# Kernel tuning notes

Measured on AMD Instinct MI355X. Metric: run time of the kernel, lower is better.

Reference implementation:

```python
import jax, jax.numpy as jnp
import numpy as np
import math

B, T, C, H = 4, 2048, 1024, 16
HD = C // H  # head dim = 64


def setup_inputs() -> dict:
    key = jax.random.key(0)
    ks = jax.random.split(key, 8)
    s = 0.02
    x = jax.random.normal(ks[0], (B, T, C), dtype=jnp.float32)
    Wq = jax.random.normal(ks[1], (C, C), dtype=jnp.float32) * s
    bq = jnp.zeros((C,), dtype=jnp.float32)
    Wkv = jax.random.normal(ks[2], (C, 2 * C), dtype=jnp.float32) * s
    bkv = jnp.zeros((2 * C,), dtype=jnp.float32)
    Wp = jax.random.normal(ks[3], (C, C), dtype=jnp.float32) * s
    bp = jnp.zeros((C,), dtype=jnp.float32)
    # ALiBi slopes: m_h = 2^(-8*(h+1)/H), shape [H,1,1] to broadcast over [B,H,T,T]
    slopes = 2.0 ** (-8.0 * (jnp.arange(1, H + 1, dtype=jnp.float32) / H))
    alibi_m = slopes.reshape(H, 1, 1)
    # relative-position offset table: offset[i,j] = -(i-j) for j<=i, 0 elsewhere
    i = jnp.arange(T)[:, None]
    j = jnp.arange(T)[None, :]
    alibi_offset = jnp.where(j <= i, (j - i).astype(jnp.float32), 0.0)
    return {"x": x, "Wq": Wq, "bq": bq, "Wkv": Wkv, "bkv": bkv,
            "Wp": Wp, "bp": bp, "alibi_m": alibi_m, "alibi_offset": alibi_offset}


def reference(x, Wq, bq, Wkv, bkv, Wp, bp, alibi_m, alibi_offset):
    Bq, Tq, Cq = x.shape
    q = x @ Wq + bq                                  # [B,T,C]
    kv = x @ Wkv + bkv                               # [B,T,2C]
    k, v = jnp.split(kv, 2, axis=-1)
    q = q.reshape(Bq, Tq, H, HD).transpose(0, 2, 1, 3)  # [B,H,T,hd]
    k = k.reshape(Bq, Tq, H, HD).transpose(0, 2, 1, 3)
    v = v.reshape(Bq, Tq, H, HD).transpose(0, 2, 1, 3)
    att = jnp.einsum('bhqd,bhkd->bhqk', q, k) / math.sqrt(HD)  # [B,H,T,T]
    att = att + alibi_m * alibi_offset[:Tq, :Tq]
    causal = jnp.tril(jnp.ones((Tq, Tq), dtype=bool))
    att = jnp.where(causal, att, -jnp.inf)
    att = jax.nn.softmax(att, axis=-1)
    y = jnp.einsum('bhqk,bhkd->bhqd', att, v)        # [B,H,T,hd]
    y = y.transpose(0, 2, 1, 3).reshape(Bq, Tq, Cq)
    y = y @ Wp + bp
    return y
```

## Files before the change

### kernel.cpp

```cpp
#include <hip/hip_runtime.h>
#include <hip/hip_bf16.h>
#include <math.h>

typedef __bf16 bf16_t;
typedef bf16_t bf16x8 __attribute__((ext_vector_type(8)));
typedef bf16_t bf16x4 __attribute__((ext_vector_type(4)));
typedef float  f32x4  __attribute__((ext_vector_type(4)));

#define MFMA_16x16x32_BF16(a, b, c) __builtin_amdgcn_mfma_f32_16x16x32_bf16((a), (b), (c), 0, 0, 0)

static constexpr int BB = 4, TT = 2048, CC = 1024, HH = 16, HD = 64;
static constexpr int C3 = 3 * CC;
static constexpr int MM = BB * TT;
static constexpr size_t SL = (size_t)BB * HH * TT * HD;

__device__ __forceinline__ float fast_exp2(float x) {
  float r;
  asm("v_exp_f32 %0, %1" : "=v"(r) : "v"(x));
  return r;
}

__device__ __forceinline__ void gload16(const void* g, void* l) {
  __builtin_amdgcn_global_load_lds(
      (const __attribute__((address_space(1))) unsigned int*)g,
      (__attribute__((address_space(3))) unsigned int*)l, 16, 0, 0);
}

__global__ void cast_x_kernel(const float* __restrict__ x, bf16_t* __restrict__ xb, int n4) {
  int i = blockIdx.x * blockDim.x + threadIdx.x;
  if (i >= n4) return;
  float4 v = reinterpret_cast<const float4*>(x)[i];
  bf16x4 o;
  o[0] = (bf16_t)v.x; o[1] = (bf16_t)v.y; o[2] = (bf16_t)v.z; o[3] = (bf16_t)v.w;
  reinterpret_cast<bf16x4*>(xb)[i] = o;
}

__global__ void transpose_cast_kernel(const float* __restrict__ in, bf16_t* __restrict__ out,
                                      int R, int Cn) {
  __shared__ float tile[32][33];
  int c0 = blockIdx.x * 32, r0 = blockIdx.y * 32;
  int tx = threadIdx.x, ty = threadIdx.y;
#pragma unroll
  for (int i = 0; i < 4; ++i)
    tile[ty + 8 * i][tx] = in[(size_t)(r0 + ty + 8 * i) * Cn + c0 + tx];
  __syncthreads();
#pragma unroll
  for (int i = 0; i < 4; ++i)
    out[(size_t)(c0 + ty + 8 * i) * R + r0 + tx] = (bf16_t)tile[tx][ty + 8 * i];
}

__global__ void transpose_v_kernel(const bf16_t* __restrict__ vh, bf16_t* __restrict__ vt) {
  __shared__ bf16_t tile[32][33];
  int t0 = blockIdx.x * 32, d0 = blockIdx.y * 32, bh = blockIdx.z;
  int tx = threadIdx.x, ty = threadIdx.y;
  const bf16_t* src = vh + (size_t)bh * TT * HD;
  bf16_t* dst = vt + (size_t)bh * TT * HD + (size_t)(t0 >> 5) * (HD * 32);
#pragma unroll
  for (int i = 0; i < 4; ++i)
    tile[ty + 8 * i][tx] = src[(size_t)(t0 + ty + 8 * i) * HD + d0 + tx];
  __syncthreads();
#pragma unroll
  for (int i = 0; i < 4; ++i)
    dst[(size_t)(d0 + ty + 8 * i) * 32 + tx] = tile[tx][ty + 8 * i];
}

__global__ void concat_bias_kernel(const float* __restrict__ bq, const float* __restrict__ bkv,
                                   float* __restrict__ dst) {
  int i = blockIdx.x * 256 + threadIdx.x;
  if (i >= 3072) return;
  const float* p = (i < 1024) ? (bq + i) : (bkv + i - 1024);
  dst[i] = *p;
}

__device__ inline void store_out(float* p, float v)  { *p = v; }
__device__ inline void store_out(bf16_t* p, float v) { *p = (bf16_t)v; }

template <int SPLIT, typename OutT>
__global__ __launch_bounds__(256) void gemm_kernel(
    const bf16_t* __restrict__ A, const bf16_t* __restrict__ Bt, OutT* __restrict__ C,
    const float* __restrict__ bias, int M, int N, int K, int gx, int cpx) {
  __shared__ bf16_t As[128][64];
  __shared__ bf16_t Bs[128][64];
  const int tid = threadIdx.x;
  const int wid = tid >> 6, lane = tid & 63;
  const int lhi = lane >> 4, llo = lane & 15;
  const int wm = (wid >> 1) * 64, wn = (wid & 1) * 64;
  const int bid = blockIdx.x;
  const int xcd = bid & 7, lb = bid >> 3;
  const int bandw = gx >> 3;
  const int bx = xcd * bandw + (lb % bandw);
  const int by = lb / bandw;
  const int m0 = bx * 128, n0 = by * 128;
  const int l8 = lane >> 3;
  const int s8 = ((lane & 7) ^ l8) * 8;

  const bf16_t* gA = A + (size_t)(m0 + wid * 32 + l8) * K + s8;
  const bf16_t* gB = Bt + (size_t)(n0 + wid * 32 + l8) * K + s8;
  bf16_t* lA = &As[wid * 32][0];
  bf16_t* lB = &Bs[wid * 32][0];
  const int rs0 = (lhi ^ (llo & 7)) * 16;

  f32x4 acc[4][4] = {};
  for (int k0 = 0; k0 < K; k0 += 64) {
    __syncthreads();
#pragma unroll
    for (int g = 0; g < 4; ++g) {
      gload16(gA + k0 + (size_t)(8 * g) * K, lA + 8 * g * 64);
      gload16(gB + k0 + (size_t)(8 * g) * K, lB + 8 * g * 64);
    }
    __syncthreads();
#pragma unroll
    for (int kk = 0; kk < 2; ++kk) {
      const int ro = rs0 ^ (kk * 64);
      bf16x8 af[4], bfr[4];
#pragma unroll
      for (int mi = 0; mi < 4; ++mi)
        af[mi] = *(const bf16x8*)((const char*)&As[wm + mi * 16 + llo][0] + ro);
#pragma unroll
      for (int ni = 0; ni < 4; ++ni)
        bfr[ni] = *(const bf16x8*)((const char*)&Bs[wn + ni * 16 + llo][0] + ro);
#pragma unroll
      for (int mi = 0; mi < 4; ++mi)
#pragma unroll
        for (int ni = 0; ni < 4; ++ni)
          acc[mi][ni] = MFMA_16x16x32_BF16(af[mi], bfr[ni], acc[mi][ni]);
    }
  }

#pragma unroll
  for (int mi = 0; mi < 4; ++mi) {
#pragma unroll
    for (int ni = 0; ni < 4; ++ni) {
      const int row0 = m0 + wm + mi * 16 + 4 * lhi;
      const int col  = n0 + wn + ni * 16 + llo;
      const float bv = bias[col];
      if constexpr (SPLIT) {
        const int sel = col >> 10, rem = col & 1023;
        const int hh = rem >> 6, dd = rem & 63;
#pragma unroll
        for (int r = 0; r < 4; ++r) {
          const int row = row0 + r;
          const int bb = row >> 11, t = row & 2047;
          size_t addr = ((((size_t)sel * BB + bb) * HH + hh) * TT + t) * HD + dd;
          ((bf16_t*)C)[addr] = (bf16_t)(acc[mi][ni][r] + bv);
        }
      } else {
#pragma unroll
        for (int r = 0; r < 4; ++r)
          store_out(&C[(size_t)(row0 + r) * N + col], acc[mi][ni][r] + bv);
      }
    }
  }
}

__global__ __launch_bounds__(256, 3) void attn_kernel(
    const bf16_t* __restrict__ qh,
    const bf16_t* __restrict__ kh,
    const bf16_t* __restrict__ vt,
    const float* __restrict__ alibi_m,
    bf16_t* __restrict__ y) {
  __shared__ bf16_t Klds[2][64][64];
  __shared__ bf16_t Vlds[2][2][64][32];
  __shared__ bf16_t Plds[4][32][68];
  const int tid = threadIdx.x, wid = tid >> 6, lane = tid & 63;
  const int lhi = lane >> 4, llo = lane & 15;
  const int bid = blockIdx.x;
  const int x = bid & 7, u = bid >> 3;
  const int b = u & 3, sel = (u >> 2) & 1, jtd = u >> 3;
  const int h = sel ? (15 - x) : x;
  const int jt = 15 - jtd;
  const int bh = b * HH + h;
  const int q0 = jt * 128 + wid * 32;

  const float mh2 = alibi_m[h] * 1.44269504f;
  const float C1 = 0.18033688f;
  const float M0 = 17.3f;
  const int Dwin = (int)(40.0f / mh2);

  const bf16_t* qbase = qh + (size_t)bh * TT * HD;
  const bf16_t* kbase = kh + (size_t)bh * TT * HD;
  const bf16_t* vbase = vt + (size_t)bh * TT * HD;

  float frm[2][4], w16c[4];
#pragma unroll
  for (int f = 0; f < 2; ++f)
#pragma unroll
    for (int r = 0; r < 4; ++r) frm[f][r] = (float)(16 * f + r) * mh2;
#pragma unroll
  for (int c = 0; c < 4; ++c) w16c[c] = fast_exp2((float)(16 * c) * mh2);

  const int l8 = lane >> 3;
  const size_t kst = (size_t)(wid * 8 + l8) * 64 + ((lane & 7) ^ l8) * 8;
  const int vf_st = ((lane >> 2) & 3) ^ ((lane >> 4) & 3);
  const size_t vst = (size_t)(wid * 16 + (lane >> 2)) * 32 + ((lane & 3) ^ vf_st) * 8;

#define STAGE(BUF, KV0)                                                          \
  do {                                                                           \
    const bf16_t* ks_ = kbase + (size_t)(KV0) * HD + kst;                        \
    bf16_t* kd_ = &Klds[BUF][0][0] + wid * 512;                                  \
    gload16(ks_, kd_);                                                           \
    gload16(ks_ + 2048, kd_ + 2048);                                             \
    const bf16_t* vs_ = vbase + ((size_t)((KV0) >> 5)) * 2048 + vst;             \
    bf16_t* vd_ = &Vlds[BUF][0][0][0] + wid * 512;                               \
    gload16(vs_, vd_);                                                           \
    gload16(vs_ + 2048, vd_ + 2048);                                             \
  } while (0)

  bf16x8 qf[2][2];
#pragma unroll
  for (int f = 0; f < 2; ++f) {
    const bf16_t* qp = qbase + (size_t)(q0 + 16 * f + llo) * HD + 8 * lhi;
    qf[f][0] = *(const bf16x8*)qp;
    qf[f][1] = *(const bf16x8*)(qp + 32);
  }

  f32x4 acc[2][4] = {};
  float lsum[2][4] = {};
  const float bias0 = mh2 * (float)(llo - 4 * lhi - q0) - M0;

  const int kvT = jt * 128;
  int ksm = kvT - Dwin; ksm = (ksm < 0) ? 0 : (ksm & ~63);
  const int nIter = (kvT - ksm) >> 6;

  if (nIter > 0) STAGE(0, ksm);
  __syncthreads();

  const int krd0 = (lhi ^ (llo & 7)) * 16;
  const int krd1 = ((4 + lhi) ^ (llo & 7)) * 16;
  const int vrd = (lhi ^ ((llo & 3) ^ ((llo >> 2) & 3))) * 16;

  int buf = 0;
#pragma unroll 1
  for (int it = 0; it < nIter; ++it) {
    const int kv0 = ksm + (it << 6);
    if (it + 1 < nIter) STAGE(buf ^ 1, kv0 + 64);
    const char* kb = (const char*)&Klds[buf][0][0];
    const char* vb = (const char*)&Vlds[buf][0][0][0];
    f32x4 s[2][4];
#pragma unroll
    for (int c = 0; c < 4; ++c) {
      bf16x8 k0 = *(const bf16x8*)(kb + (16 * c + llo) * 128 + krd0);
      bf16x8 k1 = *(const bf16x8*)(kb + (16 * c + llo) * 128 + krd1);
      s[0][c] = MFMA_16x16x32_BF16(qf[0][0], k0, f32x4{});
      s[0][c] = MFMA_16x16x32_BF16(qf[0][1], k1, s[0][c]);
      s[1][c] = MFMA_16x16x32_BF16(qf[1][0], k0, f32x4{});
      s[1][c] = MFMA_16x16x32_BF16(qf[1][1], k1, s[1][c]);
    }
    bf16x8 vv[4][2];
#pragma unroll
    for (int d = 0; d < 4; ++d) {
      vv[d][0] = *(const bf16x8*)(vb + (16 * d + llo) * 64 + vrd);
      vv[d][1] = *(const bf16x8*)(vb + 4096 + (16 * d + llo) * 64 + vrd);
    }
    const float tb0 = fmaf(mh2, (float)kv0, bias0);
#pragma unroll
    for (int f = 0; f < 2; ++f) {
#pragma unroll
      for (int r = 0; r < 4; ++r) {
        const float rb = tb0 - frm[f][r];
#pragma unroll
        for (int c = 0; c < 4; ++c) {
          float pv = fast_exp2(fmaf(s[f][c][r], C1, rb)) * w16c[c];
          lsum[f][r] += pv;
          Plds[wid][16 * f + 4 * lhi + r][16 * c + llo] = (bf16_t)pv;
        }
      }
    }
#pragma unroll
    for (int f = 0; f < 2; ++f) {
      const bf16x8 pa0 = *(const bf16x8*)&Plds[wid][16 * f + llo][8 * lhi];
      const bf16x8 pa1 = *(const bf16x8*)&Plds[wid][16 * f + llo][32 + 8 * lhi];
#pragma unroll
      for (int d = 0; d < 4; ++d) {
        acc[f][d] = MFMA_16x16x32_BF16(pa0, vv[d][0], acc[f][d]);
        acc[f][d] = MFMA_16x16x32_BF16(pa1, vv[d][1], acc[f][d]);
      }
    }
    __syncthreads();
    buf ^= 1;
  }

  const int tend = q0 & ~63;
#pragma unroll 1
  for (int kv0 = kvT; kv0 <= tend; kv0 += 64) {
    const int d31 = q0 + 31 - kv0;
    const int dbase = q0 + 4 * lhi - llo - kv0;
    f32x4 s[2][4];
#pragma unroll
    for (int c = 0; c < 4; ++c) {
      if (16 * c > d31) continue;
      const bf16_t* kp = kbase + (size_t)(kv0 + 16 * c + llo) * HD + 8 * lhi;
      bf16x8 k0 = *(const bf16x8*)kp;
      bf16x8 k1 = *(const bf16x8*)(kp + 32);
      s[0][c] = MFMA_16x16x32_BF16(qf[0][0], k0, f32x4{});
      s[0][c] = MFMA_16x16x32_BF16(qf[0][1], k1, s[0][c]);
      s[1][c] = MFMA_16x16x32_BF16(qf[1][0], k0, f32x4{});
      s[1][c] = MFMA_16x16x32_BF16(qf[1][1], k1, s[1][c]);
    }
    bf16x8 vv[4][2];
    {
      const bf16_t* vp = vbase + (size_t)(kv0 >> 5) * 2048 + (size_t)llo * 32 + 8 * lhi;
#pragma unroll
      for (int d = 0; d < 4; ++d) {
        vv[d][0] = *(const bf16x8*)(vp + d * 512);
        vv[d][1] = *(const bf16x8*)(vp + d * 512 + 2048);
      }
    }
    const float tb0 = fmaf(mh2, (float)kv0, bias0);
#pragma unroll
    for (int f = 0; f < 2; ++f) {
#pragma unroll
      for (int r = 0; r < 4; ++r) {
        const float rb = tb0 - frm[f][r];
#pragma unroll
        for (int c = 0; c < 4; ++c) {
          float pv = 0.f;
          if (16 * c <= d31) {
            pv = fast_exp2(fmaf(s[f][c][r], C1, rb)) * w16c[c];
            pv = (16 * c - 16 * f - r <= dbase) ? pv : 0.f;
            lsum[f][r] += pv;
          }
          Plds[wid][16 * f + 4 * lhi + r][16 * c + llo] = (bf16_t)pv;
        }
      }
    }
#pragma unroll
    for (int f = 0; f < 2; ++f) {
      const bf16x8 pa0 = *(const bf16x8*)&Plds[wid][16 * f + llo][8 * lhi];
      const bf16x8 pa1 = *(const bf16x8*)&Plds[wid][16 * f + llo][32 + 8 * lhi];
#pragma unroll
      for (int d = 0; d < 4; ++d) {
        acc[f][d] = MFMA_16x16x32_BF16(pa0, vv[d][0], acc[f][d]);
        acc[f][d] = MFMA_16x16x32_BF16(pa1, vv[d][1], acc[f][d]);
      }
    }
  }
#undef STAGE

#pragma unroll
  for (int f = 0; f < 2; ++f) {
    float rl[4];
#pragma unroll
    for (int r = 0; r < 4; ++r) {
#pragma unroll
      for (int off = 1; off < 16; off <<= 1)
        lsum[f][r] += __shfl_xor(lsum[f][r], off, 64);
      rl[r] = __builtin_amdgcn_rcpf(lsum[f][r]);
    }
#pragma unroll
    for (int d = 0; d < 4; ++d)
#pragma unroll
      for (int r = 0; r < 4; ++r) {
        const int row = q0 + 16 * f + 4 * lhi + r;
        y[(size_t)(b * TT + row) * CC + h * HD + 16 * d + llo] =
            (bf16_t)(acc[f][d][r] * rl[r]);
      }
  }
}

extern "C" void kernel_launch(void* const* d_in, const int* in_sizes, int n_in,
                              void* d_out, int out_size, void* d_ws, size_t ws_size,
                              hipStream_t stream) {
  const float* x       = (const float*)d_in[0];
  const float* Wq      = (const float*)d_in[1];
  const float* bq      = (const float*)d_in[2];
  const float* Wkv     = (const float*)d_in[3];
  const float* bkv     = (const float*)d_in[4];
  const float* Wp      = (const float*)d_in[5];
  const float* bp      = (const float*)d_in[6];
  const float* alibi_m = (const float*)d_in[7];
  float* out = (float*)d_out;

  char* w = (char*)d_ws;
  bf16_t* xb   = (bf16_t*)w; w += (size_t)MM * CC * 2;
  bf16_t* qkvh = (bf16_t*)w; w += SL * 3 * 2;
  bf16_t* btq  = (bf16_t*)w; w += (size_t)C3 * CC * 2;
  bf16_t* wpt  = (bf16_t*)w; w += (size_t)CC * CC * 2;
  bf16_t* vtb  = (bf16_t*)w; w += SL * 2;
  float*  bcat = (float*)w;  w += (size_t)C3 * 4;
  bf16_t* yb   = xb;

  dim3 tb(32, 8);
  cast_x_kernel<<<8192, 256, 0, stream>>>(x, xb, MM * CC / 4);
  transpose_cast_kernel<<<dim3(32, 32), tb, 0, stream>>>(Wq, btq, 1024, 1024);
  transpose_cast_kernel<<<dim3(64, 32), tb, 0, stream>>>(Wkv, btq + (size_t)1024 * 1024, 1024, 2048);
  transpose_cast_kernel<<<dim3(32, 32), tb, 0, stream>>>(Wp, wpt, 1024, 1024);
  concat_bias_kernel<<<12, 256, 0, stream>>>(bq, bkv, bcat);

  gemm_kernel<1, bf16_t><<<dim3(64 * 24), 256, 0, stream>>>(
      xb, btq, qkvh, bcat, MM, C3, CC, 64, (64 * 24) / 8);
  transpose_v_kernel<<<dim3(TT / 32, HD / 32, BB * HH), tb, 0, stream>>>(qkvh + 2 * SL, vtb);
  attn_kernel<<<dim3(1024), 256, 0, stream>>>(qkvh, qkvh + SL, vtb, alibi_m, yb);
  gemm_kernel<0, float><<<dim3(64 * 8), 256, 0, stream>>>(
      yb, wpt, out, bp, MM, CC, CC, 64, (64 * 8) / 8);
}
```

Baseline: 180.0 us.

## Fuse V transpose into QKV GEMM epilogue and enlarge GEMM tiles to 256x128

Drops the separate V-transpose kernel: the QKV GEMM epilogue now writes V directly in the blocked transposed layout the attention kernel expects, using 4-wide bf16 vector stores. Both GEMMs move to 512-thread blocks with 256x128 output tiles, so each block reuses its B tile across twice as many rows of A. This saves one kernel launch and a round trip of V through global memory. In exchange the grids shrink to 768 and 256 blocks, which may reduce occupancy and load balance on the output projection.

```diff
diff --git a/kernel.cpp b/kernel.cpp
--- a/kernel.cpp
+++ b/kernel.cpp
@@ -49,21 +49,6 @@
     out[(size_t)(c0 + ty + 8 * i) * R + r0 + tx] = (bf16_t)tile[tx][ty + 8 * i];
 }
 
-__global__ void transpose_v_kernel(const bf16_t* __restrict__ vh, bf16_t* __restrict__ vt) {
-  __shared__ bf16_t tile[32][33];
-  int t0 = blockIdx.x * 32, d0 = blockIdx.y * 32, bh = blockIdx.z;
-  int tx = threadIdx.x, ty = threadIdx.y;
-  const bf16_t* src = vh + (size_t)bh * TT * HD;
-  bf16_t* dst = vt + (size_t)bh * TT * HD + (size_t)(t0 >> 5) * (HD * 32);
-#pragma unroll
-  for (int i = 0; i < 4; ++i)
-    tile[ty + 8 * i][tx] = src[(size_t)(t0 + ty + 8 * i) * HD + d0 + tx];
-  __syncthreads();
-#pragma unroll
-  for (int i = 0; i < 4; ++i)
-    dst[(size_t)(d0 + ty + 8 * i) * 32 + tx] = tile[tx][ty + 8 * i];
-}
-
 __global__ void concat_bias_kernel(const float* __restrict__ bq, const float* __restrict__ bkv,
                                    float* __restrict__ dst) {
   int i = blockIdx.x * 256 + threadIdx.x;
@@ -76,10 +61,10 @@
 __device__ inline void store_out(bf16_t* p, float v) { *p = (bf16_t)v; }
 
 template <int SPLIT, typename OutT>
-__global__ __launch_bounds__(256) void gemm_kernel(
+__global__ __launch_bounds__(512, 2) void gemm_kernel(
     const bf16_t* __restrict__ A, const bf16_t* __restrict__ Bt, OutT* __restrict__ C,
-    const float* __restrict__ bias, int M, int N, int K, int gx, int cpx) {
-  __shared__ bf16_t As[128][64];
+    bf16_t* __restrict__ Vt, const float* __restrict__ bias, int M, int N, int K, int gx) {
+  __shared__ bf16_t As[256][64];
   __shared__ bf16_t Bs[128][64];
   const int tid = threadIdx.x;
   const int wid = tid >> 6, lane = tid & 63;
@@ -90,24 +75,25 @@
   const int bandw = gx >> 3;
   const int bx = xcd * bandw + (lb % bandw);
   const int by = lb / bandw;
-  const int m0 = bx * 128, n0 = by * 128;
+  const int m0 = bx * 256, n0 = by * 128;
   const int l8 = lane >> 3;
   const int s8 = ((lane & 7) ^ l8) * 8;
 
   const bf16_t* gA = A + (size_t)(m0 + wid * 32 + l8) * K + s8;
-  const bf16_t* gB = Bt + (size_t)(n0 + wid * 32 + l8) * K + s8;
+  const bf16_t* gB = Bt + (size_t)(n0 + wid * 16 + l8) * K + s8;
   bf16_t* lA = &As[wid * 32][0];
-  bf16_t* lB = &Bs[wid * 32][0];
+  bf16_t* lB = &Bs[wid * 16][0];
   const int rs0 = (lhi ^ (llo & 7)) * 16;
 
   f32x4 acc[4][4] = {};
   for (int k0 = 0; k0 < K; k0 += 64) {
     __syncthreads();
 #pragma unroll
-    for (int g = 0; g < 4; ++g) {
+    for (int g = 0; g < 4; ++g)
       gload16(gA + k0 + (size_t)(8 * g) * K, lA + 8 * g * 64);
+#pragma unroll
+    for (int g = 0; g < 2; ++g)
       gload16(gB + k0 + (size_t)(8 * g) * K, lB + 8 * g * 64);
-    }
     __syncthreads();
 #pragma unroll
     for (int kk = 0; kk < 2; ++kk) {
@@ -137,12 +123,19 @@
       if constexpr (SPLIT) {
         const int sel = col >> 10, rem = col & 1023;
         const int hh = rem >> 6, dd = rem & 63;
-#pragma unroll
-        for (int r = 0; r < 4; ++r) {
-          const int row = row0 + r;
-          const int bb = row >> 11, t = row & 2047;
-          size_t addr = ((((size_t)sel * BB + bb) * HH + hh) * TT + t) * HD + dd;
-          ((bf16_t*)C)[addr] = (bf16_t)(acc[mi][ni][r] + bv);
+        const int bb = row0 >> 11, t0 = row0 & 2047;
+        if (sel == 2) {
+          size_t addr = (((size_t)bb * HH + hh) * TT) * HD +
+                        (size_t)(t0 >> 5) * 2048 + (size_t)dd * 32 + (t0 & 31);
+          bf16x4 o;
+#pragma unroll
+          for (int r = 0; r < 4; ++r) o[r] = (bf16_t)(acc[mi][ni][r] + bv);
+          *(bf16x4*)&Vt[addr] = o;
+        } else {
+          size_t base = ((((size_t)sel * BB + bb) * HH + hh) * TT + t0) * HD + dd;
+#pragma unroll
+          for (int r = 0; r < 4; ++r)
+            ((bf16_t*)C)[base + (size_t)r * HD] = (bf16_t)(acc[mi][ni][r] + bv);
         }
       } else {
 #pragma unroll
@@ -387,10 +380,9 @@
   transpose_cast_kernel<<<dim3(32, 32), tb, 0, stream>>>(Wp, wpt, 1024, 1024);
   concat_bias_kernel<<<12, 256, 0, stream>>>(bq, bkv, bcat);
 
-  gemm_kernel<1, bf16_t><<<dim3(64 * 24), 256, 0, stream>>>(
-      xb, btq, qkvh, bcat, MM, C3, CC, 64, (64 * 24) / 8);
-  transpose_v_kernel<<<dim3(TT / 32, HD / 32, BB * HH), tb, 0, stream>>>(qkvh + 2 * SL, vtb);
+  gemm_kernel<1, bf16_t><<<dim3(768), 512, 0, stream>>>(
+      xb, btq, qkvh, vtb, bcat, MM, C3, CC, 32);
   attn_kernel<<<dim3(1024), 256, 0, stream>>>(qkvh, qkvh + SL, vtb, alibi_m, yb);
-  gemm_kernel<0, float><<<dim3(64 * 8), 256, 0, stream>>>(
-      yb, wpt, out, bp, MM, CC, CC, 64, (64 * 8) / 8);
-}
+  gemm_kernel<0, float><<<dim3(256), 512, 0, stream>>>(
+      yb, wpt, out, nullptr, bp, MM, CC, CC, 32);
+}
```

New measurement: 166.1 us. 1.08x faster.
